# Performance work log

Measured on AMD Instinct MI355X. Metric: run time of the kernel, lower is better.

## Reference

```python
import jax, jax.numpy as jnp
import numpy as np

B, N, D_V, D_H, D_K = 1024, 131072, 256, 256, 256


def setup_inputs() -> dict:
    key = jax.random.key(0)
    ks = jax.random.split(key, 12)
    s = 0.02
    V = jax.random.normal(ks[0], (B, D_V), dtype=jnp.float32)
    H = jax.random.normal(ks[1], (N, D_H), dtype=jnp.float32)
    batch_idx = jnp.sort(jax.random.randint(ks[2], (N,), 0, B)).astype(jnp.int32)
    Wq = jax.random.normal(ks[3], (D_K, D_V), dtype=jnp.float32) / np.sqrt(D_V)
    bq = jnp.zeros((D_K,), dtype=jnp.float32)
    Wk = jax.random.normal(ks[4], (D_K, D_H), dtype=jnp.float32) / np.sqrt(D_H)
    bk = jnp.zeros((D_K,), dtype=jnp.float32)
    Wv = jax.random.normal(ks[5], (D_V, D_H), dtype=jnp.float32) / np.sqrt(D_H)
    bv = jnp.zeros((D_V,), dtype=jnp.float32)
    Wo = jax.random.normal(ks[6], (D_V, 2 * D_V), dtype=jnp.float32) / np.sqrt(2 * D_V)
    bo = jnp.zeros((D_V,), dtype=jnp.float32)
    return {"V": V, "H": H, "batch_idx": batch_idx,
            "Wq": Wq, "bq": bq, "Wk": Wk, "bk": bk,
            "Wv": Wv, "bv": bv, "Wo": Wo, "bo": bo}


def reference(V, H, batch_idx, Wq, bq, Wk, bk, Wv, bv, Wo, bo):
    nb = V.shape[0]
    Q = V @ Wq.T + bq            # [B, d_k] one query per graph
    K = H @ Wk.T + bk            # [N, d_k]
    Vval = H @ Wv.T + bv         # [N, d_v]
    scale = 1.0 / jnp.sqrt(jnp.asarray(K.shape[-1], K.dtype))
    # ragged attention scores: each node attends to its graph's query
    scores = jnp.einsum('nd,nd->n', K, Q[batch_idx]) * scale   # [N]
    m = jax.ops.segment_max(scores, batch_idx, num_segments=nb)  # [B]
    e = jnp.exp(scores - m[batch_idx])
    denom = jax.ops.segment_sum(e, batch_idx, num_segments=nb)   # [B]
    attn = e / denom[batch_idx]                                  # [N]
    H_tilde = jax.ops.segment_sum(attn[:, None] * Vval, batch_idx, num_segments=nb)  # [B, d_v]
    U = jnp.concatenate([V, H_tilde], axis=-1)                   # [B, 2*d_v]
    out = U @ Wo.T + bo                                          # [B, d_v]
    # graphs with zero nodes pass V through unchanged
    count = jax.ops.segment_sum(jnp.ones_like(scores), batch_idx, num_segments=nb)
    return jnp.where((count > 0)[:, None], out, V)
```

## Files before the change

kernel.cpp:

```cpp
#include <hip/hip_runtime.h>
#include <math.h>

#define D 256
#define TWOD 512
#define BB 1024
#define NN 131072
#define LOG2E 1.4426950408889634f

typedef float v4f __attribute__((ext_vector_type(4)));

__device__ __forceinline__ v4f ldg_nt(const float* p, bool valid) {
  v4f z = {0.f, 0.f, 0.f, 0.f};
  if (valid) z = __builtin_nontemporal_load((const v4f*)p);
  return z;
}

__device__ __forceinline__ float dot4(v4f a, v4f b) {
  return fmaf(a.w, b.w, fmaf(a.z, b.z, fmaf(a.y, b.y, a.x * b.x)));
}

__global__ __launch_bounds__(256) void prep_kernel(
    const float* __restrict__ Wq, const float* __restrict__ bq,
    const float* __restrict__ Wk, const float* __restrict__ Wv,
    const float* __restrict__ bv, const float* __restrict__ Wo,
    const float* __restrict__ bo, const int* __restrict__ bidx,
    float* __restrict__ Mt, float* __restrict__ WfT,
    float* __restrict__ bqt, float* __restrict__ cvec,
    int* __restrict__ offs) {
  const int blk = blockIdx.x;
  const int t = threadIdx.x;
  if (blk < 64) {
    const int d0 = blk * 4;
    float a0 = 0.f, a1 = 0.f, a2 = 0.f, a3 = 0.f;
    for (int e = 0; e < D; ++e) {
      const float wk = Wk[(size_t)e * D + t];
      const float* wqr = Wq + (size_t)e * D + d0;
      a0 = fmaf(wqr[0], wk, a0);
      a1 = fmaf(wqr[1], wk, a1);
      a2 = fmaf(wqr[2], wk, a2);
      a3 = fmaf(wqr[3], wk, a3);
    }
    Mt[(size_t)(d0 + 0) * D + t] = a0;
    Mt[(size_t)(d0 + 1) * D + t] = a1;
    Mt[(size_t)(d0 + 2) * D + t] = a2;
    Mt[(size_t)(d0 + 3) * D + t] = a3;
  } else if (blk < 128) {
    const int h0 = (blk - 64) * 4;
    float a0 = 0.f, a1 = 0.f, a2 = 0.f, a3 = 0.f;
    for (int v = 0; v < D; ++v) {
      const float wo = Wo[(size_t)t * TWOD + D + v];
      const float* wvr = Wv + (size_t)v * D + h0;
      a0 = fmaf(wvr[0], wo, a0);
      a1 = fmaf(wvr[1], wo, a1);
      a2 = fmaf(wvr[2], wo, a2);
      a3 = fmaf(wvr[3], wo, a3);
    }
    WfT[(size_t)(D + h0 + 0) * D + t] = a0;
    WfT[(size_t)(D + h0 + 1) * D + t] = a1;
    WfT[(size_t)(D + h0 + 2) * D + t] = a2;
    WfT[(size_t)(D + h0 + 3) * D + t] = a3;
  } else if (blk < 144) {
    __shared__ float tile[64][65];
    const int b = blk - 128;
    const int r0 = (b >> 2) * 64, c0 = (b & 3) * 64;
    const int lane = t & 63, sr = t >> 6;
    #pragma unroll 4
    for (int rr = 0; rr < 16; ++rr) {
      const int r = rr * 4 + sr;
      tile[r][lane] = Wo[(size_t)(r0 + r) * TWOD + c0 + lane];
    }
    __syncthreads();
    #pragma unroll 4
    for (int rr = 0; rr < 16; ++rr) {
      const int r = rr * 4 + sr;
      WfT[(size_t)(c0 + r) * D + r0 + lane] = tile[lane][r];
    }
  } else if (blk == 144) {
    float a = 0.f;
    for (int e = 0; e < D; ++e)
      a = fmaf(Wk[(size_t)e * D + t], bq[e], a);
    bqt[t] = a;
  } else if (blk == 145) {
    float a = bo[t];
    for (int v = 0; v < D; ++v)
      a = fmaf(Wo[(size_t)t * TWOD + D + v], bv[v], a);
    cvec[t] = a;
  } else {
    const int i = (blk - 146) * 256 + t;
    if (i >= NN) return;
    const int b1 = bidx[i];
    const int b2 = (i + 1 < NN) ? bidx[i + 1] : BB;
    if (i == 0) {
      for (int b = 0; b <= b1; ++b) offs[b] = 0;
    }
    for (int b = b1 + 1; b <= b2; ++b) offs[b] = i + 1;
  }
}

__global__ __launch_bounds__(512) void f_kernel(
    const float* __restrict__ H, const float* __restrict__ V,
    const float* __restrict__ Mt, const float* __restrict__ bqt,
    const int* __restrict__ offs, const float* __restrict__ WfT,
    const float* __restrict__ cvec, float* __restrict__ out) {
  __shared__ __align__(16) char smem[8192 + 2048 + 4096];
  float (*partq)[2][D] = (float(*)[2][D])smem;
  float (*ss)[D] = (float(*)[D])smem;
  float (*part)[2][D] = (float(*)[2][D])smem;
  float* Vs  = (float*)(smem + 8192);
  float* Us2 = (float*)(smem + 10240);
  __shared__ float sm[8], sd[8];

  const int t = threadIdx.x;
  const int wave = t >> 6, lane = t & 63;
  const int blk = blockIdx.x;
  const int b0 = blk * 2;

  {
    const int i = t >> 8, d = t & 255;
    Vs[i * 256 + d] = V[(size_t)(b0 + i) * D + d];
  }
  __syncthreads();

  {
    v4f a0 = {0.f, 0.f, 0.f, 0.f}, a1 = a0;
    const int db = wave * 32;
    #pragma unroll 4
    for (int dd = 0; dd < 32; ++dd) {
      const int d = db + dd;
      const v4f w4 = *(const v4f*)(Mt + (size_t)d * D + lane * 4);
      a0 += w4 * Vs[0 * 256 + d];
      a1 += w4 * Vs[1 * 256 + d];
    }
    if (wave >= 4) {
      *(v4f*)&partq[wave - 4][0][lane * 4] = a0;
      *(v4f*)&partq[wave - 4][1][lane * 4] = a1;
    }
    __syncthreads();
    if (wave < 4) {
      v4f p0 = *(const v4f*)&partq[wave][0][lane * 4];
      v4f p1 = *(const v4f*)&partq[wave][1][lane * 4];
      *(v4f*)&partq[wave][0][lane * 4] = a0 + p0;
      *(v4f*)&partq[wave][1][lane * 4] = a1 + p1;
    }
  }
  __syncthreads();

  const int ib = wave >> 2, qq = wave & 3;
  const int bb = b0 + ib;
  const int start = offs[bb], end = offs[bb + 1];

  v4f q4 = *(const v4f*)(bqt + lane * 4);
  #pragma unroll
  for (int w = 0; w < 4; ++w) q4 += *(const v4f*)&partq[w][ib][lane * 4];
  __syncthreads();

  float m = -1e30f, den = 0.f;
  v4f acc = {0.f, 0.f, 0.f, 0.f};
  {
    const float SC = 0.0625f * LOG2E;
    const int odd = lane & 1;
    int n = start + qq * 2;
    v4f c0 = ldg_nt(H + (size_t)n * D + lane * 4, n < end);
    v4f c1 = ldg_nt(H + (size_t)(n + 1) * D + lane * 4, n + 1 < end);
    v4f e0 = ldg_nt(H + (size_t)(n + 8) * D + lane * 4, n + 8 < end);
    v4f e1 = ldg_nt(H + (size_t)(n + 9) * D + lane * 4, n + 9 < end);
    while (n < end) {
      const int nf = n + 16;
      v4f g0 = ldg_nt(H + (size_t)nf * D + lane * 4, nf < end);
      v4f g1 = ldg_nt(H + (size_t)(nf + 1) * D + lane * 4, nf + 1 < end);

      const float d0 = dot4(c0, q4);
      const float d1 = dot4(c1, q4);
      const float mine = odd ? d1 : d0;
      const float oth  = odd ? d0 : d1;
      float s = mine + __shfl_xor(oth, 1);
      s += __shfl_xor(s, 2);
      s += __shfl_xor(s, 4);
      s += __shfl_xor(s, 8);
      s += __shfl_xor(s, 16);
      s += __shfl_xor(s, 32);
      const float sc = (n + odd < end) ? s * SC : -1e30f;

      const float mm = fmaxf(sc, __shfl_xor(sc, 1));
      const float nm = fmaxf(m, mm);
      const float f = exp2f(m - nm);
      const float w = exp2f(sc - nm);
      const float wx = __shfl_xor(w, 1);
      const float wr0 = odd ? wx : w;
      const float wr1 = odd ? w : wx;
      den = fmaf(den, f, w + wx);
      acc = acc * f + c0 * wr0 + c1 * wr1;
      m = nm;

      c0 = e0; c1 = e1; e0 = g0; e1 = g1; n += 8;
    }
  }
  *(v4f*)&ss[wave][lane * 4] = acc;
  if (lane == 0) { sm[wave] = m; sd[wave] = den; }
  __syncthreads();

  {
    const int i = t >> 8, d = t & 255;
    const int w0 = i * 4;
    const float m0 = sm[w0], m1 = sm[w0 + 1], m2 = sm[w0 + 2], m3 = sm[w0 + 3];
    const float M = fmaxf(fmaxf(m0, m1), fmaxf(m2, m3));
    const float f0 = exp2f(m0 - M), f1 = exp2f(m1 - M);
    const float f2 = exp2f(m2 - M), f3 = exp2f(m3 - M);
    const float Dn = sd[w0] * f0 + sd[w0 + 1] * f1 + sd[w0 + 2] * f2 + sd[w0 + 3] * f3;
    const float inv = (Dn > 0.f) ? (1.f / Dn) : 0.f;
    const float sv = (ss[w0][d] * f0 + ss[w0 + 1][d] * f1 +
                      ss[w0 + 2][d] * f2 + ss[w0 + 3][d] * f3) * inv;
    Us2[d * 2 + i] = Vs[i * 256 + d];
    Us2[(D + d) * 2 + i] = sv;
  }
  __syncthreads();

  {
    v4f a0 = {0.f, 0.f, 0.f, 0.f}, a1 = a0;
    const int kb = wave * 64;
    #pragma unroll 4
    for (int kk = 0; kk < 64; ++kk) {
      const int k = kb + kk;
      const v4f w4 = *(const v4f*)(WfT + (size_t)k * D + lane * 4);
      const float2 u2 = *(const float2*)&Us2[k * 2];
      a0 += w4 * u2.x;
      a1 += w4 * u2.y;
    }
    if (wave >= 4) {
      *(v4f*)&part[wave - 4][0][lane * 4] = a0;
      *(v4f*)&part[wave - 4][1][lane * 4] = a1;
    }
    __syncthreads();
    if (wave < 4) {
      v4f p0 = *(const v4f*)&part[wave][0][lane * 4];
      v4f p1 = *(const v4f*)&part[wave][1][lane * 4];
      *(v4f*)&part[wave][0][lane * 4] = a0 + p0;
      *(v4f*)&part[wave][1][lane * 4] = a1 + p1;
    }
  }
  __syncthreads();
  {
    const int i = t >> 8, d = t & 255;
    const int bb2 = b0 + i;
    float s = cvec[d];
    #pragma unroll
    for (int w = 0; w < 4; ++w) s += part[w][i][d];
    const int c = offs[bb2 + 1] - offs[bb2];
    out[(size_t)bb2 * D + d] = (c > 0) ? s : Vs[i * 256 + d];
  }
}

extern "C" void kernel_launch(void* const* d_in, const int* in_sizes, int n_in,
                              void* d_out, int out_size, void* d_ws, size_t ws_size,
                              hipStream_t stream) {
  const float* V   = (const float*)d_in[0];
  const float* H   = (const float*)d_in[1];
  const int* bidx  = (const int*)d_in[2];
  const float* Wq  = (const float*)d_in[3];
  const float* bq  = (const float*)d_in[4];
  const float* Wk  = (const float*)d_in[5];
  const float* Wv  = (const float*)d_in[7];
  const float* bv  = (const float*)d_in[8];
  const float* Wo  = (const float*)d_in[9];
  const float* bo  = (const float*)d_in[10];
  float* out = (float*)d_out;

  float* ws  = (float*)d_ws;
  float* Mt  = ws;
  float* WfT = Mt + D * D;
  float* bqt = WfT + TWOD * D;
  float* cv  = bqt + D;
  int* offs  = (int*)(cv + D);

  hipLaunchKernelGGL(prep_kernel, dim3(658), dim3(256), 0, stream,
                     Wq, bq, Wk, Wv, bv, Wo, bo, bidx,
                     Mt, WfT, bqt, cv, offs);
  hipLaunchKernelGGL(f_kernel, dim3(BB / 2), dim3(512), 0, stream,
                     H, V, Mt, bqt, offs, WfT, cv, out);
}
```

Measured before the change: 50.60 us.

## Process four graphs per block and split-K the Wq·Wk prep product

The main kernel now handles four graphs per block instead of two, with two waves per graph streaming H. This halves the per-block re-reads of Mt and WfT. The H prefetch is issued before the query projection so the load latency overlaps that work. The prep kernel's Mt computation is split across four waves over the reduction dimension using vector loads, then reduced in shared memory. The costs are fewer waves streaming H per graph (2 instead of 4), only 256 blocks, and more LDS per block, which may reduce parallelism and occupancy for the bandwidth-bound H stream.

```diff
diff --git a/kernel.cpp b/kernel.cpp
--- a/kernel.cpp
+++ b/kernel.cpp
@@ -30,20 +30,28 @@
   const int blk = blockIdx.x;
   const int t = threadIdx.x;
   if (blk < 64) {
+    __shared__ __align__(16) float part[4][4][D];
+    const int wq = t >> 6, lane = t & 63;
     const int d0 = blk * 4;
-    float a0 = 0.f, a1 = 0.f, a2 = 0.f, a3 = 0.f;
-    for (int e = 0; e < D; ++e) {
-      const float wk = Wk[(size_t)e * D + t];
+    v4f a0 = {0.f, 0.f, 0.f, 0.f}, a1 = a0, a2 = a0, a3 = a0;
+    for (int ee = 0; ee < 64; ++ee) {
+      const int e = wq * 64 + ee;
+      const v4f wk4 = *(const v4f*)&Wk[(size_t)e * D + lane * 4];
       const float* wqr = Wq + (size_t)e * D + d0;
-      a0 = fmaf(wqr[0], wk, a0);
-      a1 = fmaf(wqr[1], wk, a1);
-      a2 = fmaf(wqr[2], wk, a2);
-      a3 = fmaf(wqr[3], wk, a3);
-    }
-    Mt[(size_t)(d0 + 0) * D + t] = a0;
-    Mt[(size_t)(d0 + 1) * D + t] = a1;
-    Mt[(size_t)(d0 + 2) * D + t] = a2;
-    Mt[(size_t)(d0 + 3) * D + t] = a3;
+      a0 += wk4 * wqr[0];
+      a1 += wk4 * wqr[1];
+      a2 += wk4 * wqr[2];
+      a3 += wk4 * wqr[3];
+    }
+    *(v4f*)&part[wq][0][lane * 4] = a0;
+    *(v4f*)&part[wq][1][lane * 4] = a1;
+    *(v4f*)&part[wq][2][lane * 4] = a2;
+    *(v4f*)&part[wq][3][lane * 4] = a3;
+    __syncthreads();
+    #pragma unroll
+    for (int r = 0; r < 4; ++r)
+      Mt[(size_t)(d0 + r) * D + t] =
+          part[0][r][t] + part[1][r][t] + part[2][r][t] + part[3][r][t];
   } else if (blk < 128) {
     const int h0 = (blk - 64) * 4;
     float a0 = 0.f, a1 = 0.f, a2 = 0.f, a3 = 0.f;
@@ -102,56 +110,80 @@
     const float* __restrict__ Mt, const float* __restrict__ bqt,
     const int* __restrict__ offs, const float* __restrict__ WfT,
     const float* __restrict__ cvec, float* __restrict__ out) {
-  __shared__ __align__(16) char smem[8192 + 2048 + 4096];
-  float (*partq)[2][D] = (float(*)[2][D])smem;
+  __shared__ __align__(16) char smem[16384 + 4096 + 8192];
+  float (*partq)[4][D] = (float(*)[4][D])smem;
   float (*ss)[D] = (float(*)[D])smem;
-  float (*part)[2][D] = (float(*)[2][D])smem;
-  float* Vs  = (float*)(smem + 8192);
-  float* Us2 = (float*)(smem + 10240);
+  float (*part)[4][D] = (float(*)[4][D])smem;
+  float* qs  = (float*)(smem + 16384);
+  float* Us2 = (float*)(smem + 20480);
   __shared__ float sm[8], sd[8];
+  __shared__ int soff[5];
 
   const int t = threadIdx.x;
   const int wave = t >> 6, lane = t & 63;
   const int blk = blockIdx.x;
-  const int b0 = blk * 2;
-
-  {
-    const int i = t >> 8, d = t & 255;
-    Vs[i * 256 + d] = V[(size_t)(b0 + i) * D + d];
-  }
-  __syncthreads();
-
-  {
-    v4f a0 = {0.f, 0.f, 0.f, 0.f}, a1 = a0;
+  const int b0 = blk * 4;
+
+  if (t < 5) soff[t] = offs[b0 + t];
+  {
+    const int d = t & 255, i0 = (t >> 8) * 2;
+    #pragma unroll
+    for (int j = 0; j < 2; ++j) {
+      const int i = i0 + j;
+      Us2[d * 4 + i] = V[(size_t)(b0 + i) * D + d];
+    }
+  }
+  __syncthreads();
+
+  const int ib = wave >> 1, ph = wave & 1;
+  const int start = soff[ib], end = soff[ib + 1];
+  int n = start + ph * 2;
+  v4f c0 = ldg_nt(H + (size_t)n * D + lane * 4, n < end);
+  v4f c1 = ldg_nt(H + (size_t)(n + 1) * D + lane * 4, n + 1 < end);
+  v4f e0 = ldg_nt(H + (size_t)(n + 4) * D + lane * 4, n + 4 < end);
+  v4f e1 = ldg_nt(H + (size_t)(n + 5) * D + lane * 4, n + 5 < end);
+
+  {
+    v4f a0 = {0.f, 0.f, 0.f, 0.f}, a1 = a0, a2 = a0, a3 = a0;
     const int db = wave * 32;
     #pragma unroll 4
     for (int dd = 0; dd < 32; ++dd) {
       const int d = db + dd;
       const v4f w4 = *(const v4f*)(Mt + (size_t)d * D + lane * 4);
-      a0 += w4 * Vs[0 * 256 + d];
-      a1 += w4 * Vs[1 * 256 + d];
+      const v4f vv = *(const v4f*)&Us2[d * 4];
+      a0 += w4 * vv.x; a1 += w4 * vv.y; a2 += w4 * vv.z; a3 += w4 * vv.w;
     }
     if (wave >= 4) {
       *(v4f*)&partq[wave - 4][0][lane * 4] = a0;
       *(v4f*)&partq[wave - 4][1][lane * 4] = a1;
+      *(v4f*)&partq[wave - 4][2][lane * 4] = a2;
+      *(v4f*)&partq[wave - 4][3][lane * 4] = a3;
     }
     __syncthreads();
     if (wave < 4) {
       v4f p0 = *(const v4f*)&partq[wave][0][lane * 4];
       v4f p1 = *(const v4f*)&partq[wave][1][lane * 4];
+      v4f p2 = *(const v4f*)&partq[wave][2][lane * 4];
+      v4f p3 = *(const v4f*)&partq[wave][3][lane * 4];
       *(v4f*)&partq[wave][0][lane * 4] = a0 + p0;
       *(v4f*)&partq[wave][1][lane * 4] = a1 + p1;
-    }
-  }
-  __syncthreads();
-
-  const int ib = wave >> 2, qq = wave & 3;
-  const int bb = b0 + ib;
-  const int start = offs[bb], end = offs[bb + 1];
-
-  v4f q4 = *(const v4f*)(bqt + lane * 4);
-  #pragma unroll
-  for (int w = 0; w < 4; ++w) q4 += *(const v4f*)&partq[w][ib][lane * 4];
+      *(v4f*)&partq[wave][2][lane * 4] = a2 + p2;
+      *(v4f*)&partq[wave][3][lane * 4] = a3 + p3;
+    }
+  }
+  __syncthreads();
+  {
+    const int k = t & 255, i0 = (t >> 8) * 2;
+    #pragma unroll
+    for (int j = 0; j < 2; ++j) {
+      const int i = i0 + j;
+      qs[i * 256 + k] = bqt[k] + partq[0][i][k] + partq[1][i][k] +
+                        partq[2][i][k] + partq[3][i][k];
+    }
+  }
+  __syncthreads();
+
+  const v4f q4 = *(const v4f*)&qs[ib * 256 + lane * 4];
   __syncthreads();
 
   float m = -1e30f, den = 0.f;
@@ -159,15 +191,10 @@
   {
     const float SC = 0.0625f * LOG2E;
     const int odd = lane & 1;
-    int n = start + qq * 2;
-    v4f c0 = ldg_nt(H + (size_t)n * D + lane * 4, n < end);
-    v4f c1 = ldg_nt(H + (size_t)(n + 1) * D + lane * 4, n + 1 < end);
-    v4f e0 = ldg_nt(H + (size_t)(n + 8) * D + lane * 4, n + 8 < end);
-    v4f e1 = ldg_nt(H + (size_t)(n + 9) * D + lane * 4, n + 9 < end);
     while (n < end) {
-      const int nf = n + 16;
-      v4f g0 = ldg_nt(H + (size_t)nf * D + lane * 4, nf < end);
-      v4f g1 = ldg_nt(H + (size_t)(nf + 1) * D + lane * 4, nf + 1 < end);
+      const int nn = n + 8;
+      v4f g0 = ldg_nt(H + (size_t)nn * D + lane * 4, nn < end);
+      v4f g1 = ldg_nt(H + (size_t)(nn + 1) * D + lane * 4, nn + 1 < end);
 
       const float d0 = dot4(c0, q4);
       const float d1 = dot4(c1, q4);
@@ -192,7 +219,7 @@
       acc = acc * f + c0 * wr0 + c1 * wr1;
       m = nm;
 
-      c0 = e0; c1 = e1; e0 = g0; e1 = g1; n += 8;
+      c0 = e0; c1 = e1; e0 = g0; e1 = g1; n += 4;
     }
   }
   *(v4f*)&ss[wave][lane * 4] = acc;
@@ -200,53 +227,62 @@
   __syncthreads();
 
   {
-    const int i = t >> 8, d = t & 255;
-    const int w0 = i * 4;
-    const float m0 = sm[w0], m1 = sm[w0 + 1], m2 = sm[w0 + 2], m3 = sm[w0 + 3];
-    const float M = fmaxf(fmaxf(m0, m1), fmaxf(m2, m3));
-    const float f0 = exp2f(m0 - M), f1 = exp2f(m1 - M);
-    const float f2 = exp2f(m2 - M), f3 = exp2f(m3 - M);
-    const float Dn = sd[w0] * f0 + sd[w0 + 1] * f1 + sd[w0 + 2] * f2 + sd[w0 + 3] * f3;
-    const float inv = (Dn > 0.f) ? (1.f / Dn) : 0.f;
-    const float sv = (ss[w0][d] * f0 + ss[w0 + 1][d] * f1 +
-                      ss[w0 + 2][d] * f2 + ss[w0 + 3][d] * f3) * inv;
-    Us2[d * 2 + i] = Vs[i * 256 + d];
-    Us2[(D + d) * 2 + i] = sv;
-  }
-  __syncthreads();
-
-  {
-    v4f a0 = {0.f, 0.f, 0.f, 0.f}, a1 = a0;
+    const int d = t & 255, i0 = (t >> 8) * 2;
+    #pragma unroll
+    for (int j = 0; j < 2; ++j) {
+      const int i = i0 + j;
+      const int w0 = 2 * i;
+      const float m0 = sm[w0], m1 = sm[w0 + 1];
+      const float M = fmaxf(m0, m1);
+      const float f0 = exp2f(m0 - M), f1 = exp2f(m1 - M);
+      const float Dn = sd[w0] * f0 + sd[w0 + 1] * f1;
+      const float inv = (Dn > 0.f) ? (1.f / Dn) : 0.f;
+      Us2[(D + d) * 4 + i] = (ss[w0][d] * f0 + ss[w0 + 1][d] * f1) * inv;
+    }
+  }
+  __syncthreads();
+
+  {
+    v4f a0 = {0.f, 0.f, 0.f, 0.f}, a1 = a0, a2 = a0, a3 = a0;
     const int kb = wave * 64;
     #pragma unroll 4
     for (int kk = 0; kk < 64; ++kk) {
       const int k = kb + kk;
       const v4f w4 = *(const v4f*)(WfT + (size_t)k * D + lane * 4);
-      const float2 u2 = *(const float2*)&Us2[k * 2];
-      a0 += w4 * u2.x;
-      a1 += w4 * u2.y;
+      const v4f u4 = *(const v4f*)&Us2[k * 4];
+      a0 += w4 * u4.x; a1 += w4 * u4.y; a2 += w4 * u4.z; a3 += w4 * u4.w;
     }
     if (wave >= 4) {
       *(v4f*)&part[wave - 4][0][lane * 4] = a0;
       *(v4f*)&part[wave - 4][1][lane * 4] = a1;
+      *(v4f*)&part[wave - 4][2][lane * 4] = a2;
+      *(v4f*)&part[wave - 4][3][lane * 4] = a3;
     }
     __syncthreads();
     if (wave < 4) {
       v4f p0 = *(const v4f*)&part[wave][0][lane * 4];
       v4f p1 = *(const v4f*)&part[wave][1][lane * 4];
+      v4f p2 = *(const v4f*)&part[wave][2][lane * 4];
+      v4f p3 = *(const v4f*)&part[wave][3][lane * 4];
       *(v4f*)&part[wave][0][lane * 4] = a0 + p0;
       *(v4f*)&part[wave][1][lane * 4] = a1 + p1;
-    }
-  }
-  __syncthreads();
-  {
-    const int i = t >> 8, d = t & 255;
-    const int bb2 = b0 + i;
-    float s = cvec[d];
-    #pragma unroll
-    for (int w = 0; w < 4; ++w) s += part[w][i][d];
-    const int c = offs[bb2 + 1] - offs[bb2];
-    out[(size_t)bb2 * D + d] = (c > 0) ? s : Vs[i * 256 + d];
+      *(v4f*)&part[wave][2][lane * 4] = a2 + p2;
+      *(v4f*)&part[wave][3][lane * 4] = a3 + p3;
+    }
+  }
+  __syncthreads();
+  {
+    const int d = t & 255, i0 = (t >> 8) * 2;
+    #pragma unroll
+    for (int j = 0; j < 2; ++j) {
+      const int i = i0 + j;
+      const int bb2 = b0 + i;
+      float s = cvec[d];
+      #pragma unroll
+      for (int w = 0; w < 4; ++w) s += part[w][i][d];
+      const int c = soff[i + 1] - soff[i];
+      out[(size_t)bb2 * D + d] = (c > 0) ? s : Us2[d * 4 + i];
+    }
   }
 }
 
@@ -275,6 +311,6 @@
   hipLaunchKernelGGL(prep_kernel, dim3(658), dim3(256), 0, stream,
                      Wq, bq, Wk, Wv, bv, Wo, bo, bidx,
                      Mt, WfT, bqt, cv, offs);
-  hipLaunchKernelGGL(f_kernel, dim3(BB / 2), dim3(512), 0, stream,
+  hipLaunchKernelGGL(f_kernel, dim3(BB / 4), dim3(512), 0, stream,
                      H, V, Mt, bqt, offs, WfT, cv, out);
 }
```

New measurement: 51.62 us. 1.02x slower.
